# Performance work log

Hardware: AMD Instinct MI355X
Metric: run time of the kernel (lower is better)

## Reference

```python
import jax, jax.numpy as jnp
import numpy as np

N, E, D_IN, H, D_HEAD = 50000, 800000, 128, 8, 16
SCALE = float(np.sqrt(D_HEAD))


def setup_inputs() -> dict:
    key = jax.random.key(0)
    ks = jax.random.split(key, 9)
    h = jax.random.normal(ks[0], (N, D_IN), dtype=jnp.float32)
    # Q/K/V projection params (torch Linear: y = x @ W.T + b; store as [D_IN, H*D_HEAD])
    s = 1.0 / np.sqrt(D_IN)
    Wq = jax.random.uniform(ks[1], (D_IN, H * D_HEAD), minval=-s, maxval=s, dtype=jnp.float32)
    Wk = jax.random.uniform(ks[2], (D_IN, H * D_HEAD), minval=-s, maxval=s, dtype=jnp.float32)
    Wv = jax.random.uniform(ks[3], (D_IN, H * D_HEAD), minval=-s, maxval=s, dtype=jnp.float32)
    bq = jax.random.uniform(ks[4], (H * D_HEAD,), minval=-s, maxval=s, dtype=jnp.float32)
    bk = jax.random.uniform(ks[5], (H * D_HEAD,), minval=-s, maxval=s, dtype=jnp.float32)
    bv = jax.random.uniform(ks[6], (H * D_HEAD,), minval=-s, maxval=s, dtype=jnp.float32)
    src = jax.random.randint(ks[7], (E,), 0, N, dtype=jnp.int32)
    dst = jax.random.randint(ks[8], (E,), 0, N, dtype=jnp.int32)
    return {"h": h, "Wq": Wq, "bq": bq, "Wk": Wk, "bk": bk, "Wv": Wv, "bv": bv,
            "src": src, "dst": dst}


def reference(h, Wq, bq, Wk, bk, Wv, bv, src, dst):
    n = h.shape[0]
    Q = (h @ Wq + bq).reshape(n, H, D_HEAD)
    K = (h @ Wk + bk).reshape(n, H, D_HEAD)
    V = (h @ Wv + bv).reshape(n, H, D_HEAD)
    # per-edge dot-product score: (K_src * Q_dst).sum(-1), clamped exp
    score = jnp.sum(K[src] * Q[dst], axis=-1, keepdims=True)  # [E, H, 1]
    score = jnp.exp(jnp.clip(score / SCALE, -5.0, 5.0))
    # segment-sum weighted aggregation to destination nodes
    wV = jax.ops.segment_sum(V[src] * score, dst, num_segments=n)   # [N, H, D_HEAD]
    z = jax.ops.segment_sum(score, dst, num_segments=n)              # [N, H, 1]
    return wV / (z + 1e-6)
```

## Files before the change

### kernel.cpp

```cpp
#include <hip/hip_runtime.h>
#include <hip/hip_bf16.h>

#define N_NODES 50000
#define N_EDGES 800000
#define DIN     128
#define HD      128
#define NHEAD   8
#define DHEAD   16

#define BUCKET  64
#define M_PAD   50176
#define HIST_BLOCKS  3125
#define CVTW_BLOCKS  192
#define PROJ3_BLOCKS 1173
#define SCAT_BLOCKS  3125
#define AGG_BLOCKS   12500

typedef __attribute__((ext_vector_type(8))) short short8;
typedef __attribute__((ext_vector_type(4))) float float4v;

static __device__ __forceinline__ unsigned short f2bf_bits(float f) {
    __hip_bfloat16 b = __float2bfloat16(f);
    return *reinterpret_cast<unsigned short*>(&b);
}
static __device__ __forceinline__ float bfb(short b) {
    return __uint_as_float(((unsigned int)(unsigned short)b) << 16);
}
static __device__ __forceinline__ short8 cvt8(const float* p) {
    const float4 f0 = *(const float4*)p;
    const float4 f1 = *(const float4*)(p + 4);
    short8 r;
    r[0] = (short)f2bf_bits(f0.x); r[1] = (short)f2bf_bits(f0.y);
    r[2] = (short)f2bf_bits(f0.z); r[3] = (short)f2bf_bits(f0.w);
    r[4] = (short)f2bf_bits(f1.x); r[5] = (short)f2bf_bits(f1.y);
    r[6] = (short)f2bf_bits(f1.z); r[7] = (short)f2bf_bits(f1.w);
    return r;
}

__global__ __launch_bounds__(256) void hist_cvtw_kernel(
    const int* __restrict__ dst,
    const float* __restrict__ Wq, const float* __restrict__ Wk,
    const float* __restrict__ Wv,
    int* __restrict__ counts, int* __restrict__ rank,
    unsigned short* __restrict__ Wt)
{
    const int bid = blockIdx.x;
    if (bid < HIST_BLOCKS) {
        const int e = bid * 256 + threadIdx.x;
        if (e < N_EDGES) rank[e] = atomicAdd(&counts[dst[e]], 1);
    } else {
        const int i   = (bid - HIST_BLOCKS) * 256 + threadIdx.x;
        const int n   = i & 127;
        const int k   = (i >> 7) & 127;
        const int mat = i >> 14;
        const float* W = (mat == 0) ? Wq : (mat == 1) ? Wk : Wv;
        Wt[mat * (DIN * HD) + n * DIN + k] = f2bf_bits(W[k * HD + n]);
    }
}

__global__ __launch_bounds__(256) void proj_scatter_kernel(
    const float* __restrict__ h,
    const unsigned short* __restrict__ Wt,
    const float* __restrict__ bq, const float* __restrict__ bk,
    const float* __restrict__ bv,
    const int* __restrict__ src, const int* __restrict__ dst,
    const int* __restrict__ rank,
    __hip_bfloat16* __restrict__ Qb, __hip_bfloat16* __restrict__ KV,
    int* __restrict__ sorted_src)
{
    const int bid = blockIdx.x;
    if (bid >= PROJ3_BLOCKS) {
        const int e = (bid - PROJ3_BLOCKS) * 256 + threadIdx.x;
        if (e < N_EDGES) {
            sorted_src[dst[e] * BUCKET + rank[e]] = src[e];
        }
        return;
    }

    const int mat  = bid % 3;
    const int tile = bid / 3;

    __shared__ unsigned short wlds[DIN * HD];
    {
        const unsigned short* wg = Wt + mat * (DIN * HD);
        #pragma unroll
        for (int it = 0; it < 8; ++it) {
            const int idx = it * 256 + threadIdx.x;
            const int row = idx >> 4;
            const int ch  = idx & 15;
            const int cu  = ((ch >> 2) * 8 + (row >> 4)) * 64
                          + (ch & 3) * 16 + (row & 15);
            *(short8*)&wlds[cu * 8] = *(const short8*)(wg + idx * 8);
        }
    }
    __syncthreads();

    const int wave = threadIdx.x >> 6;
    const int lane = threadIdx.x & 63;
    const int quad = lane >> 4;
    const int l16  = lane & 15;
    const int rowBase = tile * 128 + wave * 32;

    int r0 = rowBase + l16;       if (r0 >= N_NODES) r0 = N_NODES - 1;
    int r1 = rowBase + 16 + l16;  if (r1 >= N_NODES) r1 = N_NODES - 1;

    short8 afr[2][4];
    #pragma unroll
    for (int kc = 0; kc < 4; ++kc) {
        const int ko = kc * 32 + quad * 8;
        afr[0][kc] = cvt8(h + (size_t)r0 * DIN + ko);
        afr[1][kc] = cvt8(h + (size_t)r1 * DIN + ko);
    }

    const float* bias = (mat == 0) ? bq : (mat == 1) ? bk : bv;

    float4v acc[2][8];
    #pragma unroll
    for (int rt = 0; rt < 2; ++rt)
        #pragma unroll
        for (int ct = 0; ct < 8; ++ct)
            acc[rt][ct] = (float4v){0.f, 0.f, 0.f, 0.f};

    #pragma unroll
    for (int kc = 0; kc < 4; ++kc) {
        #pragma unroll
        for (int ct = 0; ct < 8; ++ct) {
            const int cu = (kc * 8 + ct) * 64 + lane;
            const short8 b = *(const short8*)&wlds[cu * 8];
            acc[0][ct] = __builtin_amdgcn_mfma_f32_16x16x32_bf16(afr[0][kc], b, acc[0][ct], 0, 0, 0);
            acc[1][ct] = __builtin_amdgcn_mfma_f32_16x16x32_bf16(afr[1][kc], b, acc[1][ct], 0, 0, 0);
        }
    }

    #pragma unroll
    for (int ct = 0; ct < 8; ++ct) {
        const int col = ct * 16 + l16;
        const float bcol = bias[col];
        #pragma unroll
        for (int rt = 0; rt < 2; ++rt) {
            #pragma unroll
            for (int r = 0; r < 4; ++r) {
                const int row = rowBase + rt * 16 + quad * 4 + r;
                if (row < N_NODES) {
                    const float v = acc[rt][ct][r] + bcol;
                    if (mat == 0)
                        Qb[(size_t)row * HD + col] = __float2bfloat16(v);
                    else
                        KV[(size_t)row * 256 + (mat == 2 ? 128 : 0) + col] =
                            __float2bfloat16(v);
                }
            }
        }
    }
}

__global__ __launch_bounds__(256) void aggregate_kernel(
    const __hip_bfloat16* __restrict__ Qb, const __hip_bfloat16* __restrict__ KV,
    const int* __restrict__ counts,
    const int* __restrict__ sorted_src, float* __restrict__ out)
{
    const int w    = threadIdx.x >> 6;
    const int node = blockIdx.x * 4 + w;
    const int lane = threadIdx.x & 63;
    const int quad = lane >> 4;
    const int l16  = lane & 15;
    const int hB   = lane >> 3;

    const int beg = node * BUCKET;
    const int end = beg + counts[node];

    __shared__ float sc_s[4][2][16][9];
    __shared__ int   s_s[4][2][16];

    const short* qrow = (const short*)Qb + (size_t)node * HD;
    const short8 zero8 = {0, 0, 0, 0, 0, 0, 0, 0};
    short8 bfr[4];
    #pragma unroll
    for (int kc = 0; kc < 4; ++kc) {
        const int head = kc * 2 + (quad >> 1);
        const short8 qv = *(const short8*)(qrow + quad * 8 + kc * 32);
        bfr[kc] = (l16 == head) ? qv : zero8;
    }

    const short* kvb = (const short*)KV;
    float acc0 = 0.f, acc1 = 0.f, zacc = 0.f;

    int buf = 0;
    for (int e0 = beg; e0 < end; e0 += 16, buf ^= 1) {
        const int nb = min(16, end - e0);

        const int eidx = e0 + l16;
        const int s = (eidx < end) ? sorted_src[eidx] : 0;
        if (quad == 0) s_s[w][buf][l16] = s;

        const short* kp = kvb + (size_t)s * 256 + quad * 8;
        float4v acc4 = {0.f, 0.f, 0.f, 0.f};
        #pragma unroll
        for (int kc = 0; kc < 4; ++kc) {
            const short8 a = *(const short8*)(kp + kc * 32);
            acc4 = __builtin_amdgcn_mfma_f32_16x16x32_bf16(a, bfr[kc], acc4, 0, 0, 0);
        }
        if (l16 < 8) {
            #pragma unroll
            for (int r = 0; r < 4; ++r) {
                const float d = acc4[r] * 0.25f;
                sc_s[w][buf][quad * 4 + r][l16] =
                    __expf(fminf(fmaxf(d, -5.f), 5.f));
            }
        }
        __threadfence_block();

        int j = 0;
        for (; j + 3 < nb; j += 4) {
            const int s0 = s_s[w][buf][j],     s1 = s_s[w][buf][j + 1];
            const int s2 = s_s[w][buf][j + 2], s3 = s_s[w][buf][j + 3];
            const float c0 = sc_s[w][buf][j][hB],     c1 = sc_s[w][buf][j + 1][hB];
            const float c2 = sc_s[w][buf][j + 2][hB], c3 = sc_s[w][buf][j + 3][hB];
            const unsigned int v0 = *(const unsigned int*)(kvb + (size_t)s0 * 256 + 128 + 2 * lane);
            const unsigned int v1 = *(const unsigned int*)(kvb + (size_t)s1 * 256 + 128 + 2 * lane);
            const unsigned int v2 = *(const unsigned int*)(kvb + (size_t)s2 * 256 + 128 + 2 * lane);
            const unsigned int v3 = *(const unsigned int*)(kvb + (size_t)s3 * 256 + 128 + 2 * lane);
            acc0 = fmaf(__uint_as_float(v0 << 16), c0, acc0);
            acc1 = fmaf(__uint_as_float(v0 & 0xffff0000u), c0, acc1);
            acc0 = fmaf(__uint_as_float(v1 << 16), c1, acc0);
            acc1 = fmaf(__uint_as_float(v1 & 0xffff0000u), c1, acc1);
            acc0 = fmaf(__uint_as_float(v2 << 16), c2, acc0);
            acc1 = fmaf(__uint_as_float(v2 & 0xffff0000u), c2, acc1);
            acc0 = fmaf(__uint_as_float(v3 << 16), c3, acc0);
            acc1 = fmaf(__uint_as_float(v3 & 0xffff0000u), c3, acc1);
            zacc += (c0 + c1) + (c2 + c3);
        }
        for (; j < nb; ++j) {
            const int s0 = s_s[w][buf][j];
            const float c0 = sc_s[w][buf][j][hB];
            const unsigned int v0 = *(const unsigned int*)(kvb + (size_t)s0 * 256 + 128 + 2 * lane);
            acc0 = fmaf(__uint_as_float(v0 << 16), c0, acc0);
            acc1 = fmaf(__uint_as_float(v0 & 0xffff0000u), c0, acc1);
            zacc += c0;
        }
    }

    const float inv = 1.f / (zacc + 1e-6f);
    float2 o;
    o.x = acc0 * inv;
    o.y = acc1 * inv;
    *(float2*)(out + (size_t)node * HD + 2 * lane) = o;
}

extern "C" void kernel_launch(void* const* d_in, const int* in_sizes, int n_in,
                              void* d_out, int out_size, void* d_ws, size_t ws_size,
                              hipStream_t stream)
{
    const float* h   = (const float*)d_in[0];
    const float* Wq  = (const float*)d_in[1];
    const float* bq  = (const float*)d_in[2];
    const float* Wk  = (const float*)d_in[3];
    const float* bk  = (const float*)d_in[4];
    const float* Wv  = (const float*)d_in[5];
    const float* bv  = (const float*)d_in[6];
    const int*   src = (const int*)d_in[7];
    const int*   dst = (const int*)d_in[8];
    float* out = (float*)d_out;

    __hip_bfloat16* Qb = (__hip_bfloat16*)d_ws;
    __hip_bfloat16* KV = Qb + (size_t)N_NODES * HD;
    unsigned short* Wt = (unsigned short*)(KV + (size_t)N_NODES * 256);
    int* counts     = (int*)(Wt + 3 * DIN * HD);
    int* sorted_src = counts + M_PAD;
    int* rank       = sorted_src + (size_t)N_NODES * BUCKET;

    hipMemsetAsync(counts, 0, M_PAD * sizeof(int), stream);

    hist_cvtw_kernel<<<HIST_BLOCKS + CVTW_BLOCKS, 256, 0, stream>>>(
        dst, Wq, Wk, Wv, counts, rank, Wt);

    proj_scatter_kernel<<<PROJ3_BLOCKS + SCAT_BLOCKS, 256, 0, stream>>>(
        h, Wt, bq, bk, bv, src, dst, rank, Qb, KV, sorted_src);

    aggregate_kernel<<<AGG_BLOCKS, 256, 0, stream>>>(
        Qb, KV, counts, sorted_src, out);
}
```

Before: 226.0 us.

## Zero counts in-kernel and co-schedule histogram atomics with projection GEMM

Replaces the memset with zeroing blocks merged into the weight-conversion kernel. The histogram atomics now run inside the projection kernel, overlapping the atomic-bound edge pass with the GEMM blocks, and the scatter moves to its own kernel. This removes a memset launch and hides the histogram latency behind compute, but adds a separate scatter launch and leaves the scatter no longer overlapped with projection.

```diff
diff --git a/kernel.cpp b/kernel.cpp
--- a/kernel.cpp
+++ b/kernel.cpp
@@ -10,9 +10,10 @@
 
 #define BUCKET  64
 #define M_PAD   50176
-#define HIST_BLOCKS  3125
+#define ZERO_BLOCKS  196
 #define CVTW_BLOCKS  192
 #define PROJ3_BLOCKS 1173
+#define HIST_BLOCKS  3125
 #define SCAT_BLOCKS  3125
 #define AGG_BLOCKS   12500
 
@@ -37,19 +38,16 @@
     return r;
 }
 
-__global__ __launch_bounds__(256) void hist_cvtw_kernel(
-    const int* __restrict__ dst,
+__global__ __launch_bounds__(256) void zero_cvtw_kernel(
     const float* __restrict__ Wq, const float* __restrict__ Wk,
     const float* __restrict__ Wv,
-    int* __restrict__ counts, int* __restrict__ rank,
-    unsigned short* __restrict__ Wt)
+    int* __restrict__ counts, unsigned short* __restrict__ Wt)
 {
     const int bid = blockIdx.x;
-    if (bid < HIST_BLOCKS) {
-        const int e = bid * 256 + threadIdx.x;
-        if (e < N_EDGES) rank[e] = atomicAdd(&counts[dst[e]], 1);
+    if (bid < ZERO_BLOCKS) {
+        counts[bid * 256 + threadIdx.x] = 0;
     } else {
-        const int i   = (bid - HIST_BLOCKS) * 256 + threadIdx.x;
+        const int i   = (bid - ZERO_BLOCKS) * 256 + threadIdx.x;
         const int n   = i & 127;
         const int k   = (i >> 7) & 127;
         const int mat = i >> 14;
@@ -58,22 +56,19 @@
     }
 }
 
-__global__ __launch_bounds__(256) void proj_scatter_kernel(
+__global__ __launch_bounds__(256) void proj_hist_kernel(
     const float* __restrict__ h,
     const unsigned short* __restrict__ Wt,
     const float* __restrict__ bq, const float* __restrict__ bk,
     const float* __restrict__ bv,
-    const int* __restrict__ src, const int* __restrict__ dst,
-    const int* __restrict__ rank,
-    __hip_bfloat16* __restrict__ Qb, __hip_bfloat16* __restrict__ KV,
-    int* __restrict__ sorted_src)
+    const int* __restrict__ dst,
+    int* __restrict__ counts, int* __restrict__ rank,
+    __hip_bfloat16* __restrict__ Qb, __hip_bfloat16* __restrict__ KV)
 {
     const int bid = blockIdx.x;
     if (bid >= PROJ3_BLOCKS) {
         const int e = (bid - PROJ3_BLOCKS) * 256 + threadIdx.x;
-        if (e < N_EDGES) {
-            sorted_src[dst[e] * BUCKET + rank[e]] = src[e];
-        }
+        if (e < N_EDGES) rank[e] = atomicAdd(&counts[dst[e]], 1);
         return;
     }
 
@@ -152,6 +147,14 @@
             }
         }
     }
+}
+
+__global__ __launch_bounds__(256) void scatter_kernel(
+    const int* __restrict__ src, const int* __restrict__ dst,
+    const int* __restrict__ rank, int* __restrict__ sorted_src)
+{
+    const int e = blockIdx.x * 256 + threadIdx.x;
+    if (e < N_EDGES) sorted_src[dst[e] * BUCKET + rank[e]] = src[e];
 }
 
 __global__ __launch_bounds__(256) void aggregate_kernel(
@@ -269,13 +272,14 @@
     int* sorted_src = counts + M_PAD;
     int* rank       = sorted_src + (size_t)N_NODES * BUCKET;
 
-    hipMemsetAsync(counts, 0, M_PAD * sizeof(int), stream);
-
-    hist_cvtw_kernel<<<HIST_BLOCKS + CVTW_BLOCKS, 256, 0, stream>>>(
-        dst, Wq, Wk, Wv, counts, rank, Wt);
-
-    proj_scatter_kernel<<<PROJ3_BLOCKS + SCAT_BLOCKS, 256, 0, stream>>>(
-        h, Wt, bq, bk, bv, src, dst, rank, Qb, KV, sorted_src);
+    zero_cvtw_kernel<<<ZERO_BLOCKS + CVTW_BLOCKS, 256, 0, stream>>>(
+        Wq, Wk, Wv, counts, Wt);
+
+    proj_hist_kernel<<<PROJ3_BLOCKS + HIST_BLOCKS, 256, 0, stream>>>(
+        h, Wt, bq, bk, bv, dst, counts, rank, Qb, KV);
+
+    scatter_kernel<<<SCAT_BLOCKS, 256, 0, stream>>>(
+        src, dst, rank, sorted_src);
 
     aggregate_kernel<<<AGG_BLOCKS, 256, 0, stream>>>(
         Qb, KV, counts, sorted_src, out);
```

After: 216.0 us. 4.4% less time.
